# Kernel optimization log

Hardware: AMD Instinct MI355X
Metric: run time of the kernel (lower is better)

The kernel has to match this reference:

```python
import jax, jax.numpy as jnp
import numpy as np

N, D, K = 65536, 256, 4096
EPS = 1e-5
DECAY = 0.99
BN_MOMENTUM = 0.1


def setup_inputs() -> dict:
    key = jax.random.key(0)
    k1, k2, k3, k4, k5, k6 = jax.random.split(key, 6)
    return {
        "x": jax.random.normal(k1, (N, D), dtype=jnp.float32),
        "embedding": jax.random.normal(k2, (K, D), dtype=jnp.float32),
        "ema_cluster_size": jnp.zeros((K,), dtype=jnp.float32),
        "ema_w": jax.random.normal(k3, (K, D), dtype=jnp.float32),
        "running_mean": jax.random.normal(k4, (D,), dtype=jnp.float32) * 0.1,
        "running_var": jax.random.uniform(k5, (D,), dtype=jnp.float32, minval=0.5, maxval=1.5),
    }


def reference(x, embedding, ema_cluster_size, ema_w, running_mean, running_var):
    n_batch = x.shape[0]
    num_embeddings = embedding.shape[0]

    # BatchNorm1d (training mode, affine=False): normalize with batch stats
    mean = jnp.mean(x, axis=0)                       # [D]
    var = jnp.mean((x - mean) ** 2, axis=0)          # biased var, [D]
    xn = (x - mean) / jnp.sqrt(var + EPS)            # [N, D]
    # running stat updates (torch uses unbiased var for running_var)
    new_running_mean = (1.0 - BN_MOMENTUM) * running_mean + BN_MOMENTUM * mean
    var_unbiased = var * (n_batch / (n_batch - 1.0))
    new_running_var = (1.0 - BN_MOMENTUM) * running_var + BN_MOMENTUM * var_unbiased

    # squared euclidean distances [N, K]
    distances = (jnp.sum(xn ** 2, axis=1, keepdims=True)
                 + jnp.sum(embedding ** 2, axis=1)
                 - 2.0 * xn @ embedding.T)
    idx = jnp.argmin(distances, axis=1)              # [N]

    # one-hot scatter stats via segment_sum (== encodings.T contractions)
    counts = jax.ops.segment_sum(jnp.ones((n_batch,), dtype=x.dtype), idx,
                                 num_segments=num_embeddings)   # [K]
    dw = jax.ops.segment_sum(xn, idx, num_segments=num_embeddings)  # [K, D]

    # EMA updates
    new_cs = ema_cluster_size * DECAY + (1.0 - DECAY) * counts
    n_total = jnp.sum(new_cs)
    new_cs = (new_cs + 1e-5) / (n_total + num_embeddings * 1e-5) * n_total
    new_ema_w = ema_w * DECAY + (1.0 - DECAY) * dw
    new_embedding = new_ema_w / new_cs[:, None]

    running_std = jnp.sqrt(new_running_var + EPS)
    embedding_output = new_embedding * running_std[None, :] + new_running_mean[None, :]

    return (idx[:, None], new_embedding, embedding_output, new_cs, new_ema_w,
            new_running_mean, new_running_var)
```

## Files before the change

kernel.cpp:

```cpp
#include <hip/hip_runtime.h>
#include <cfloat>
#include <cmath>

#define NROWS 65536
#define DDIM 256
#define KDIM 4096

typedef short bf16x8 __attribute__((ext_vector_type(8)));
typedef float f32x4 __attribute__((ext_vector_type(4)));

constexpr float EPSV = 1e-5f;
constexpr float DECAYV = 0.99f;
constexpr float MOMV = 0.1f;
constexpr float DELTA = 0.5f;
constexpr int CAP = 16;
constexpr int SEG = 128;

constexpr size_t WS_CNT     = 0;
constexpr size_t WS_NFLAG   = WS_CNT + NROWS;
constexpr size_t WS_HIST    = WS_NFLAG + 64;
constexpr size_t WS_ZEND    = WS_HIST + KDIM;
constexpr size_t WS_START   = WS_ZEND;
constexpr size_t WS_FILLPOS = WS_START + KDIM;
constexpr size_t WS_SEGSTART= WS_FILLPOS + KDIM;
constexpr size_t WS_NSEG    = WS_SEGSTART + KDIM + 64;
constexpr size_t WS_SEGLIST = WS_NSEG + 64;
constexpr size_t WS_PARTSUM = WS_SEGLIST + 4672;
constexpr size_t WS_PARTSQ  = WS_PARTSUM + 2048 * DDIM;
constexpr size_t WS_MIDSUM  = WS_PARTSQ + 2048 * DDIM;
constexpr size_t WS_MIDSQ   = WS_MIDSUM + 256 * DDIM;
constexpr size_t WS_MEAN    = WS_MIDSQ + 256 * DDIM;
constexpr size_t WS_RSTD    = WS_MEAN + DDIM;
constexpr size_t WS_NRMEAN  = WS_RSTD + DDIM;
constexpr size_t WS_NRVAR   = WS_NRMEAN + DDIM;
constexpr size_t WS_BVEC    = WS_NRVAR + DDIM;
constexpr size_t WS_NCSRAW  = WS_BVEC + KDIM;
constexpr size_t WS_NTOT    = WS_NCSRAW + KDIM;
constexpr size_t WS_ROWINFO = WS_NTOT + 64;
constexpr size_t WS_IDX     = WS_ROWINFO + 8 * (size_t)NROWS;
constexpr size_t WS_ROWTHR  = WS_IDX + NROWS;
constexpr size_t WS_FLAG    = WS_ROWTHR + NROWS;
constexpr size_t WS_ROWLIST = WS_FLAG + NROWS;
constexpr size_t WS_CAND    = WS_ROWLIST + NROWS;
constexpr size_t WS_DWPART  = WS_CAND;
constexpr size_t WS_EPROW   = WS_CAND + (size_t)NROWS * CAP;
constexpr size_t WS_EIMG    = WS_EPROW + (size_t)KDIM * DDIM;
constexpr size_t WS_XIMG    = WS_EIMG + 524288;

constexpr size_t O_IDX   = 0;
constexpr size_t O_EMB   = NROWS;
constexpr size_t O_EOUT  = O_EMB + (size_t)KDIM * DDIM;
constexpr size_t O_CS    = O_EOUT + (size_t)KDIM * DDIM;
constexpr size_t O_EMAW  = O_CS + KDIM;
constexpr size_t O_RMEAN = O_EMAW + (size_t)KDIM * DDIM;
constexpr size_t O_RVAR  = O_RMEAN + DDIM;

__device__ inline unsigned bfpack(float a, float b) {
    unsigned ua = __float_as_uint(a), ub = __float_as_uint(b);
    ua = (ua + 0x7FFFu + ((ua >> 16) & 1u)) >> 16;
    ub = (ub + 0x7FFFu + ((ub >> 16) & 1u)) & 0xFFFF0000u;
    return (ua & 0xFFFFu) | ub;
}

__device__ inline float unpackval(float p) {
    return __uint_as_float(__float_as_uint(p) & 0xFFFFF000u);
}

#define GLOAD_LDS16(g, l) __builtin_amdgcn_global_load_lds(                       \
        (const __attribute__((address_space(1))) void*)(g),                        \
        (__attribute__((address_space(3))) void*)(l), 16, 0, 0)

__global__ __launch_bounds__(256) void k_bnpack(const float* __restrict__ x,
                                                float* __restrict__ ws) {
    const int t = threadIdx.x;
    const int q = t & 63, g = t >> 6;
    const int r0 = blockIdx.x * 128 + g * 32;
    char* ximg = (char*)(ws + WS_XIMG);
    const float4* x4 = (const float4*)x;
    float4 s = make_float4(0.f, 0.f, 0.f, 0.f);
    float4 sq = make_float4(0.f, 0.f, 0.f, 0.f);
#pragma unroll 4
    for (int i = 0; i < 32; ++i) {
        const int r = r0 + i;
        const float4 v = x4[(size_t)r * 64 + q];
        s.x += v.x; s.y += v.y; s.z += v.z; s.w += v.w;
        sq.x += v.x * v.x; sq.y += v.y * v.y; sq.z += v.z * v.z; sq.w += v.w * v.w;
        const int db = (8 * q + ((r & 15) << 5)) & 511;
        *(uint2*)(ximg + (size_t)r * 512 + db) = make_uint2(bfpack(v.x, v.y), bfpack(v.z, v.w));
    }
    const size_t p = (size_t)(blockIdx.x * 4 + g) * 64 + q;
    ((float4*)(ws + WS_PARTSUM))[p] = s;
    ((float4*)(ws + WS_PARTSQ))[p]  = sq;
}

__global__ __launch_bounds__(256) void k_bn_mid(float* __restrict__ ws) {
    const int d = threadIdx.x, j = blockIdx.x;
    float s = 0.f, q = 0.f;
#pragma unroll
    for (int i = 0; i < 8; ++i) {
        s += ws[WS_PARTSUM + (size_t)(j * 8 + i) * DDIM + d];
        q += ws[WS_PARTSQ  + (size_t)(j * 8 + i) * DDIM + d];
    }
    ws[WS_MIDSUM + (size_t)j * DDIM + d] = s;
    ws[WS_MIDSQ  + (size_t)j * DDIM + d] = q;
}

__global__ __launch_bounds__(256) void k_bn_final(const float* __restrict__ rmean_in,
                                                  const float* __restrict__ rvar_in,
                                                  float* __restrict__ ws,
                                                  float* __restrict__ out) {
    const int d = threadIdx.x;
    float s = 0.f, sq = 0.f;
    for (int b = 0; b < 256; ++b) {
        s  += ws[WS_MIDSUM + (size_t)b * DDIM + d];
        sq += ws[WS_MIDSQ  + (size_t)b * DDIM + d];
    }
    const float mean = s / (float)NROWS;
    float var = sq / (float)NROWS - mean * mean;
    var = fmaxf(var, 0.f);
    const float rstd = 1.0f / sqrtf(var + EPSV);
    const float nrm  = (1.0f - MOMV) * rmean_in[d] + MOMV * mean;
    const float varu = var * ((float)NROWS / (float)(NROWS - 1));
    const float nrv  = (1.0f - MOMV) * rvar_in[d] + MOMV * varu;
    ws[WS_MEAN + d] = mean;
    ws[WS_RSTD + d] = rstd;
    ws[WS_NRMEAN + d] = nrm;
    ws[WS_NRVAR + d] = nrv;
    out[O_RMEAN + d] = nrm;
    out[O_RVAR + d] = nrv;
}

__global__ __launch_bounds__(256) void k_eprime(const float* __restrict__ emb,
                                                float* __restrict__ ws) {
    const int t = threadIdx.x, l = t & 63, w = t >> 6;
    const int k = blockIdx.x * 4 + w;
    const float4 em = ((const float4*)emb)[(size_t)k * 64 + l];
    const float4 rs = ((const float4*)(ws + WS_RSTD))[l];
    const float4 mn = ((const float4*)(ws + WS_MEAN))[l];
    float4 e;
    e.x = em.x * rs.x; e.y = em.y * rs.y; e.z = em.z * rs.z; e.w = em.w * rs.w;
    ((float4*)(ws + WS_EPROW))[(size_t)k * 64 + l] = e;
    char* img = (char*)(ws + WS_EIMG);
    const int db = (8 * l + ((k & 15) << 5)) & 511;
    *(uint2*)(img + (size_t)k * 512 + db) =
        make_uint2(bfpack(-2.f * e.x, -2.f * e.y), bfpack(-2.f * e.z, -2.f * e.w));
    float red = em.x * em.x + 2.f * mn.x * e.x + em.y * em.y + 2.f * mn.y * e.y
              + em.z * em.z + 2.f * mn.z * e.z + em.w * em.w + 2.f * mn.w * e.w;
    red += __shfl_xor(red, 32); red += __shfl_xor(red, 16); red += __shfl_xor(red, 8);
    red += __shfl_xor(red, 4);  red += __shfl_xor(red, 2);  red += __shfl_xor(red, 1);
    if (l == 0) ws[WS_BVEC + k] = red;
}

__global__ __launch_bounds__(256, 4) void k_gemm_min(float* __restrict__ ws) {
    extern __shared__ char smem[];
    const int t = threadIdx.x, lane = t & 63, w = t >> 6;
    const int l4 = lane & 15, kg = lane >> 4;
    const int tile = blockIdx.x >> 2;
    const int cq   = blockIdx.x & 3;
    const int rowbase = tile * 128 + w * 32;
    const char* ximg = (const char*)(ws + WS_XIMG);
    const char* eimg = (const char*)(ws + WS_EIMG) + (size_t)cq * 524288;
    const float* bvec = ws + WS_BVEC;

    bf16x8 a[2][8];
#pragma unroll
    for (int m = 0; m < 2; ++m) {
        const char* rp = ximg + (size_t)(rowbase + m * 16 + l4) * 512;
#pragma unroll
        for (int ts = 0; ts < 8; ++ts) {
            const int byte = ((kg * 16 + ts * 64) + (l4 << 5)) & 511;
            a[m][ts] = *(const bf16x8*)(rp + byte);
        }
    }

    float b1f[2][4], b2f[2][4];
#pragma unroll
    for (int m = 0; m < 2; ++m)
#pragma unroll
        for (int r = 0; r < 4; ++r) { b1f[m][r] = FLT_MAX; b2f[m][r] = FLT_MAX; }

#pragma unroll
    for (int rr = 0; rr < 4; ++rr) {
        const int off = rr * 4096 + w * 1024;
        GLOAD_LDS16(eimg + off + lane * 16, smem + off);
    }
    float bc0 = bvec[cq * 1024 + l4];
    float bc1 = bvec[cq * 1024 + 16 + l4];
    __syncthreads();

    for (int ch = 0; ch < 32; ++ch) {
        const char* cur = smem + (ch & 1) * 16384;
        float bn0 = 0.f, bn1 = 0.f;
        if (ch + 1 < 32) {
            const char* src = eimg + (size_t)(ch + 1) * 16384;
            char* nb = smem + ((ch + 1) & 1) * 16384;
#pragma unroll
            for (int rr = 0; rr < 4; ++rr) {
                const int off = rr * 4096 + w * 1024;
                GLOAD_LDS16(src + off + lane * 16, nb + off);
            }
            bn0 = bvec[cq * 1024 + (ch + 1) * 32 + l4];
            bn1 = bvec[cq * 1024 + (ch + 1) * 32 + 16 + l4];
        }

        f32x4 acc[2][2];
        acc[0][0] = (f32x4){bc0, bc0, bc0, bc0};
        acc[0][1] = (f32x4){bc1, bc1, bc1, bc1};
        acc[1][0] = acc[0][0];
        acc[1][1] = acc[0][1];

#pragma unroll
        for (int ts = 0; ts < 8; ++ts) {
            const int rot = ((kg * 16 + ts * 64) + (l4 << 5)) & 511;
            bf16x8 bfr[2];
#pragma unroll
            for (int n = 0; n < 2; ++n)
                bfr[n] = *(const bf16x8*)(cur + (n * 16 + l4) * 512 + rot);
#pragma unroll
            for (int m = 0; m < 2; ++m)
#pragma unroll
                for (int n = 0; n < 2; ++n)
                    acc[m][n] = __builtin_amdgcn_mfma_f32_16x16x32_bf16(a[m][ts], bfr[n], acc[m][n], 0, 0, 0);
        }

#pragma unroll
        for (int n = 0; n < 2; ++n) {
            const unsigned col = (unsigned)(cq * 1024 + ch * 32 + n * 16 + l4);
#pragma unroll
            for (int m = 0; m < 2; ++m)
#pragma unroll
                for (int r = 0; r < 4; ++r) {
                    const float p = __uint_as_float(
                        (__float_as_uint(acc[m][n][r]) & 0xFFFFF000u) | col);
                    b2f[m][r] = __builtin_amdgcn_fmed3f(p, b1f[m][r], b2f[m][r]);
                    b1f[m][r] = fminf(p, b1f[m][r]);
                }
        }
        bc0 = bn0; bc1 = bn1;
        __syncthreads();
    }

    float2* rowinfo = (float2*)(ws + WS_ROWINFO);
#pragma unroll
    for (int m = 0; m < 2; ++m)
#pragma unroll
        for (int r = 0; r < 4; ++r) {
            float v1 = b1f[m][r], v2 = b2f[m][r];
#pragma unroll
            for (int st = 1; st < 16; st <<= 1) {
                const float o1 = __shfl_xor(v1, st);
                const float o2 = __shfl_xor(v2, st);
                const float mm = fminf(v2, o2);
                v2 = __builtin_amdgcn_fmed3f(v1, o1, mm);
                v1 = fminf(v1, o1);
            }
            if (l4 == 0) {
                const int row = rowbase + m * 16 + kg * 4 + r;
                rowinfo[(size_t)row * 4 + cq] = make_float2(v1, v2);
            }
        }
}

__global__ __launch_bounds__(256) void k_flag(float* __restrict__ ws,
                                              float* __restrict__ out) {
    const int r = blockIdx.x * 256 + threadIdx.x;
    const float2* rowinfo = (const float2*)(ws + WS_ROWINFO);
    float2 q = rowinfo[(size_t)r * 4];
    float v1 = q.x, v2 = q.y;
#pragma unroll
    for (int c = 1; c < 4; ++c) {
        q = rowinfo[(size_t)r * 4 + c];
        const float mm = fminf(v2, q.y);
        v2 = __builtin_amdgcn_fmed3f(v1, q.x, mm);
        v1 = fminf(v1, q.x);
    }
    const float v1v = unpackval(v1);
    const int   i1  = (int)(__float_as_uint(v1) & 0xFFFu);
    ws[WS_ROWTHR + r] = v1v + DELTA;
    if (unpackval(v2) - v1v <= DELTA) {
        const int pos = atomicAdd((int*)(ws + WS_NFLAG), 1);
        ((int*)(ws + WS_FLAG))[pos] = r;
    } else {
        out[O_IDX + r] = (float)i1;
        ((int*)(ws + WS_IDX))[r] = i1;
        atomicAdd((int*)(ws + WS_HIST) + i1, 1);
    }
}

__global__ __launch_bounds__(256) void k_cand(float* __restrict__ ws) {
    extern __shared__ char smem[];
    const int t = threadIdx.x, lane = t & 63, w = t >> 6;
    const int l4 = lane & 15, kg = lane >> 4;
    const char* ximg = (const char*)(ws + WS_XIMG);
    const char* eimg0 = (const char*)(ws + WS_EIMG);
    const float* bvec = ws + WS_BVEC;
    const int* flag = (const int*)(ws + WS_FLAG);
    int* cnt = (int*)(ws + WS_CNT);
    int* cand = (int*)(ws + WS_CAND);
    const int nflag = *(const int*)(ws + WS_NFLAG);
    if (nflag == 0) return;
    const int ntiles = (nflag + 127) >> 7;
    const int nitems = ntiles * 8;

    for (int item = blockIdx.x; item < nitems; item += gridDim.x) {
        const int tile = item >> 3, slice = item & 7;
        const int base = tile * 128 + w * 32;
        const char* eimg = eimg0 + (size_t)slice * 262144;
        bf16x8 a[2][8];
        int frow[2][4];
        float thr[2][4];
#pragma unroll
        for (int m = 0; m < 2; ++m) {
            const int ia = base + m * 16 + l4;
            const int rowa = flag[ia < nflag ? ia : (nflag - 1)];
            const char* rp = ximg + (size_t)rowa * 512;
#pragma unroll
            for (int ts = 0; ts < 8; ++ts) {
                const int byte = ((kg * 16 + ts * 64) + ((rowa & 15) << 5)) & 511;
                a[m][ts] = *(const bf16x8*)(rp + byte);
            }
#pragma unroll
            for (int r = 0; r < 4; ++r) {
                const int ie = base + m * 16 + kg * 4 + r;
                const bool val = ie < nflag;
                const int rowe = flag[val ? ie : (nflag - 1)];
                frow[m][r] = rowe;
                thr[m][r] = val ? ws[WS_ROWTHR + rowe] : -FLT_MAX;
            }
        }
#pragma unroll
        for (int rr = 0; rr < 4; ++rr) {
            const int off = rr * 4096 + w * 1024;
            GLOAD_LDS16(eimg + off + lane * 16, smem + off);
        }
        __syncthreads();

        for (int ch = 0; ch < 16; ++ch) {
            const char* cur = smem + (ch & 1) * 16384;
            if (ch + 1 < 16) {
                const char* src = eimg + (size_t)(ch + 1) * 16384;
                char* nb = smem + ((ch + 1) & 1) * 16384;
#pragma unroll
                for (int rr = 0; rr < 4; ++rr) {
                    const int off = rr * 4096 + w * 1024;
                    GLOAD_LDS16(src + off + lane * 16, nb + off);
                }
            }
            const float bc0 = bvec[slice * 512 + ch * 32 + l4];
            const float bc1 = bvec[slice * 512 + ch * 32 + 16 + l4];
            f32x4 acc[2][2];
            acc[0][0] = (f32x4){bc0, bc0, bc0, bc0};
            acc[0][1] = (f32x4){bc1, bc1, bc1, bc1};
            acc[1][0] = acc[0][0];
            acc[1][1] = acc[0][1];
#pragma unroll
            for (int ts = 0; ts < 8; ++ts) {
                const int rot = ((kg * 16 + ts * 64) + (l4 << 5)) & 511;
                bf16x8 bfr[2];
#pragma unroll
                for (int n = 0; n < 2; ++n)
                    bfr[n] = *(const bf16x8*)(cur + (n * 16 + l4) * 512 + rot);
#pragma unroll
                for (int m = 0; m < 2; ++m)
#pragma unroll
                    for (int n = 0; n < 2; ++n)
                        acc[m][n] = __builtin_amdgcn_mfma_f32_16x16x32_bf16(a[m][ts], bfr[n], acc[m][n], 0, 0, 0);
            }
#pragma unroll
            for (int n = 0; n < 2; ++n) {
                const int col = slice * 512 + ch * 32 + n * 16 + l4;
#pragma unroll
                for (int m = 0; m < 2; ++m)
#pragma unroll
                    for (int r = 0; r < 4; ++r) {
                        const float s = acc[m][n][r];
                        if (s <= thr[m][r]) {
                            const int rr2 = frow[m][r];
                            const int pos = atomicAdd(&cnt[rr2], 1);
                            if (pos < CAP) cand[(size_t)rr2 * CAP + pos] = col;
                        }
                    }
            }
            __syncthreads();
        }
    }
}

__global__ __launch_bounds__(256) void k_resolve_f(const float* __restrict__ x,
                                                   float* __restrict__ ws,
                                                   float* __restrict__ out) {
    const int t = threadIdx.x, lane = t & 63;
    const int gw = (blockIdx.x * 256 + t) >> 6;
    const int nflag = *(const int*)(ws + WS_NFLAG);
    const int* flag = (const int*)(ws + WS_FLAG);
    const int* cnt = (const int*)(ws + WS_CNT);
    const int* cand = (const int*)(ws + WS_CAND);
    const float* eprow = ws + WS_EPROW;
    const float* bvec = ws + WS_BVEC;
    int* idx_int = (int*)(ws + WS_IDX);
    for (int i = gw; i < nflag; i += 1024) {
        const int row = flag[i];
        const float4 xr = ((const float4*)(x + (size_t)row * DDIM))[lane];
        const int n = cnt[row];
        float bestv = FLT_MAX;
        int bestk = KDIM;
        if (n >= 1 && n <= CAP) {
            for (int c = 0; c < n; ++c) {
                const int k = cand[(size_t)row * CAP + c];
                const float4 er = ((const float4*)(eprow + (size_t)k * DDIM))[lane];
                float p = xr.x * er.x + xr.y * er.y + xr.z * er.z + xr.w * er.w;
                p += __shfl_xor(p, 32); p += __shfl_xor(p, 16); p += __shfl_xor(p, 8);
                p += __shfl_xor(p, 4);  p += __shfl_xor(p, 2);  p += __shfl_xor(p, 1);
                const float s = fmaf(-2.f, p, bvec[k]);
                if (s < bestv || (s == bestv && k < bestk)) { bestv = s; bestk = k; }
            }
        } else {
            for (int k = 0; k < KDIM; ++k) {
                const float4 er = ((const float4*)(eprow + (size_t)k * DDIM))[lane];
                float p = xr.x * er.x + xr.y * er.y + xr.z * er.z + xr.w * er.w;
                p += __shfl_xor(p, 32); p += __shfl_xor(p, 16); p += __shfl_xor(p, 8);
                p += __shfl_xor(p, 4);  p += __shfl_xor(p, 2);  p += __shfl_xor(p, 1);
                const float s = fmaf(-2.f, p, bvec[k]);
                if (s < bestv || (s == bestv && k < bestk)) { bestv = s; bestk = k; }
            }
        }
        if (lane == 0) {
            out[O_IDX + row] = (float)bestk;
            idx_int[row] = bestk;
            atomicAdd((int*)(ws + WS_HIST) + bestk, 1);
        }
    }
}

__global__ __launch_bounds__(256) void k_scan(const float* __restrict__ cs_in,
                                              float* __restrict__ ws) {
    __shared__ int lsum[256], lseg[256];
    __shared__ float redf[256];
    const int t = threadIdx.x;
    const int* hist = (const int*)(ws + WS_HIST);
    int h[16];
    int s = 0, g = 0;
#pragma unroll
    for (int i = 0; i < 16; ++i) {
        h[i] = hist[t * 16 + i];
        s += h[i];
        g += (h[i] + SEG - 1) / SEG;
    }
    lsum[t] = s; lseg[t] = g;
    __syncthreads();
    int v = s, u = g;
    for (int off = 1; off < 256; off <<= 1) {
        const int av = (t >= off) ? lsum[t - off] : 0;
        const int au = (t >= off) ? lseg[t - off] : 0;
        __syncthreads();
        v += av; u += au;
        lsum[t] = v; lseg[t] = u;
        __syncthreads();
    }
    int runs = v - s, rung = u - g;
    int* start = (int*)(ws + WS_START);
    int* fillpos = (int*)(ws + WS_FILLPOS);
    int* segst = (int*)(ws + WS_SEGSTART);
    int* seglist = (int*)(ws + WS_SEGLIST);
    float emapart = 0.f;
#pragma unroll
    for (int i = 0; i < 16; ++i) {
        const int k = t * 16 + i;
        start[k] = runs;
        fillpos[k] = runs;
        segst[k] = rung;
        const int ns = (h[i] + SEG - 1) / SEG;
        for (int j = 0; j < ns; ++j) seglist[rung + j] = (k << 10) | j;
        runs += h[i];
        rung += ns;
        const float ncs = cs_in[k] * DECAYV + (1.0f - DECAYV) * (float)h[i];
        ws[WS_NCSRAW + k] = ncs;
        emapart += ncs;
    }
    if (t == 255) {
        segst[KDIM] = rung;
        *(int*)(ws + WS_NSEG) = rung;
    }
    redf[t] = emapart;
    __syncthreads();
    for (int ss = 128; ss > 0; ss >>= 1) { if (t < ss) redf[t] += redf[t + ss]; __syncthreads(); }
    if (t == 0) ws[WS_NTOT] = redf[0];
}

__global__ __launch_bounds__(256) void k_fill(float* __restrict__ ws) {
    const int r = blockIdx.x * 256 + threadIdx.x;
    const int k = ((const int*)(ws + WS_IDX))[r];
    const int pos = atomicAdd((int*)(ws + WS_FILLPOS) + k, 1);
    ((int*)(ws + WS_ROWLIST))[pos] = r;
}

__global__ __launch_bounds__(256) void k_gather_seg(const float* __restrict__ x,
                                                    float* __restrict__ ws) {
    __shared__ float4 ls[4][64];
    const int b = blockIdx.x;
    if (b >= *(const int*)(ws + WS_NSEG)) return;
    const int e = ((const int*)(ws + WS_SEGLIST))[b];
    const int k = e >> 10, j = e & 1023;
    const int base = ((const int*)(ws + WS_START))[k];
    const int n = ((const int*)(ws + WS_HIST))[k];
    const int st = base + j * SEG;
    const int en = min(st + SEG, base + n);
    const int* rowlist = (const int*)(ws + WS_ROWLIST);
    const int t = threadIdx.x, q = t & 63, g = t >> 6;
    const float4* x4 = (const float4*)x;
    float4 s = make_float4(0.f, 0.f, 0.f, 0.f);
    for (int i = st + g; i < en; i += 4) {
        const float4 v = x4[(size_t)rowlist[i] * 64 + q];
        s.x += v.x; s.y += v.y; s.z += v.z; s.w += v.w;
    }
    ls[g][q] = s;
    __syncthreads();
    if (t < 64) {
        const float4 a0 = ls[0][t], a1 = ls[1][t], a2 = ls[2][t], a3 = ls[3][t];
        float4 r;
        r.x = (a0.x + a1.x) + (a2.x + a3.x);
        r.y = (a0.y + a1.y) + (a2.y + a3.y);
        r.z = (a0.z + a1.z) + (a2.z + a3.z);
        r.w = (a0.w + a1.w) + (a2.w + a3.w);
        ((float4*)(ws + WS_DWPART))[(size_t)b * 64 + t] = r;
    }
}

__global__ __launch_bounds__(64) void k_final(const float* __restrict__ ema_w,
                                              const float* __restrict__ ws,
                                              float* __restrict__ out) {
    const int k = blockIdx.x;
    const int q = threadIdx.x;
    const int* segst = (const int*)(ws + WS_SEGSTART);
    const int ss = segst[k];
    const int ns = segst[k + 1] - ss;
    const float4* dwpart = (const float4*)(ws + WS_DWPART);
    float4 a = make_float4(0.f, 0.f, 0.f, 0.f);
    for (int j = 0; j < ns; ++j) {
        const float4 v = dwpart[(size_t)(ss + j) * 64 + q];
        a.x += v.x; a.y += v.y; a.z += v.z; a.w += v.w;
    }
    const int n = ((const int*)(ws + WS_HIST))[k];
    const float ntot = ws[WS_NTOT];
    const float ncs  = (ws[WS_NCSRAW + k] + 1e-5f) / (ntot + (float)KDIM * 1e-5f) * ntot;
    const float4 mn = ((const float4*)(ws + WS_MEAN))[q];
    const float4 rs = ((const float4*)(ws + WS_RSTD))[q];
    const float4 nrv = ((const float4*)(ws + WS_NRVAR))[q];
    const float4 nrm = ((const float4*)(ws + WS_NRMEAN))[q];
    const float4 ew = ((const float4*)ema_w)[(size_t)k * 64 + q];
    const float fn = (float)n;
    float4 nwv, nembv, eov;
    nwv.x = ew.x * DECAYV + (1.f - DECAYV) * ((a.x - fn * mn.x) * rs.x);
    nwv.y = ew.y * DECAYV + (1.f - DECAYV) * ((a.y - fn * mn.y) * rs.y);
    nwv.z = ew.z * DECAYV + (1.f - DECAYV) * ((a.z - fn * mn.z) * rs.z);
    nwv.w = ew.w * DECAYV + (1.f - DECAYV) * ((a.w - fn * mn.w) * rs.w);
    const float inv = 1.0f / ncs;
    nembv.x = nwv.x * inv; nembv.y = nwv.y * inv;
    nembv.z = nwv.z * inv; nembv.w = nwv.w * inv;
    eov.x = nembv.x * sqrtf(nrv.x + EPSV) + nrm.x;
    eov.y = nembv.y * sqrtf(nrv.y + EPSV) + nrm.y;
    eov.z = nembv.z * sqrtf(nrv.z + EPSV) + nrm.z;
    eov.w = nembv.w * sqrtf(nrv.w + EPSV) + nrm.w;
    ((float4*)(out + O_EMB))[(size_t)k * 64 + q]  = nembv;
    ((float4*)(out + O_EOUT))[(size_t)k * 64 + q] = eov;
    ((float4*)(out + O_EMAW))[(size_t)k * 64 + q] = nwv;
    if (q == 0) out[O_CS + k] = ncs;
}

extern "C" void kernel_launch(void* const* d_in, const int* in_sizes, int n_in,
                              void* d_out, int out_size, void* d_ws, size_t ws_size,
                              hipStream_t stream) {
    const float* x     = (const float*)d_in[0];
    const float* emb   = (const float*)d_in[1];
    const float* cs    = (const float*)d_in[2];
    const float* ema_w = (const float*)d_in[3];
    const float* rmean = (const float*)d_in[4];
    const float* rvar  = (const float*)d_in[5];
    float* out = (float*)d_out;
    float* ws  = (float*)d_ws;

    hipMemsetAsync(ws, 0, WS_ZEND * sizeof(float), stream);

    k_bnpack<<<512, 256, 0, stream>>>(x, ws);
    k_bn_mid<<<256, 256, 0, stream>>>(ws);
    k_bn_final<<<1, 256, 0, stream>>>(rmean, rvar, ws, out);
    k_eprime<<<KDIM / 4, 256, 0, stream>>>(emb, ws);

    constexpr int LDSB = 32768;
    k_gemm_min<<<2048, 256, LDSB, stream>>>(ws);
    k_flag<<<NROWS / 256, 256, 0, stream>>>(ws, out);
    k_cand<<<512, 256, LDSB, stream>>>(ws);
    k_resolve_f<<<256, 256, 0, stream>>>(x, ws, out);

    k_scan<<<1, 256, 0, stream>>>(cs, ws);
    k_fill<<<NROWS / 256, 256, 0, stream>>>(ws);
    k_gather_seg<<<4608, 256, 0, stream>>>(x, ws);
    k_final<<<KDIM, 64, 0, stream>>>(ema_w, ws, out);
}
```

Measured before the change: 308.7 us.

## Read codebook fragments straight from global memory and fold BN partial reduction into pack

The GEMM-argmin kernel no longer double-buffers codebook chunks through LDS with global_load_lds and per-chunk barriers. Each wave now reads its B fragments directly from global memory and relies on cache reuse, and launch bounds drop from 4 to 3 blocks per CU. Separately, the batch-norm partial sums are reduced across the four waves inside k_bnpack through shared memory, so the k_bn_mid launch goes away and k_bn_final sums 512 partials. The trade is removing LDS traffic and synchronization in the GEMM at the risk of higher global/L2 load latency on the hot path, which may stall the MFMAs.

```diff
diff --git a/kernel.cpp b/kernel.cpp
--- a/kernel.cpp
+++ b/kernel.cpp
@@ -26,10 +26,8 @@
 constexpr size_t WS_NSEG    = WS_SEGSTART + KDIM + 64;
 constexpr size_t WS_SEGLIST = WS_NSEG + 64;
 constexpr size_t WS_PARTSUM = WS_SEGLIST + 4672;
-constexpr size_t WS_PARTSQ  = WS_PARTSUM + 2048 * DDIM;
-constexpr size_t WS_MIDSUM  = WS_PARTSQ + 2048 * DDIM;
-constexpr size_t WS_MIDSQ   = WS_MIDSUM + 256 * DDIM;
-constexpr size_t WS_MEAN    = WS_MIDSQ + 256 * DDIM;
+constexpr size_t WS_PARTSQ  = WS_PARTSUM + 512 * DDIM;
+constexpr size_t WS_MEAN    = WS_PARTSQ + 512 * DDIM;
 constexpr size_t WS_RSTD    = WS_MEAN + DDIM;
 constexpr size_t WS_NRMEAN  = WS_RSTD + DDIM;
 constexpr size_t WS_NRVAR   = WS_NRMEAN + DDIM;
@@ -72,6 +70,7 @@
 
 __global__ __launch_bounds__(256) void k_bnpack(const float* __restrict__ x,
                                                 float* __restrict__ ws) {
+    __shared__ float4 lsum[4][64], lsq[4][64];
     const int t = threadIdx.x;
     const int q = t & 63, g = t >> 6;
     const int r0 = blockIdx.x * 128 + g * 32;
@@ -88,21 +87,19 @@
         const int db = (8 * q + ((r & 15) << 5)) & 511;
         *(uint2*)(ximg + (size_t)r * 512 + db) = make_uint2(bfpack(v.x, v.y), bfpack(v.z, v.w));
     }
-    const size_t p = (size_t)(blockIdx.x * 4 + g) * 64 + q;
-    ((float4*)(ws + WS_PARTSUM))[p] = s;
-    ((float4*)(ws + WS_PARTSQ))[p]  = sq;
-}
-
-__global__ __launch_bounds__(256) void k_bn_mid(float* __restrict__ ws) {
-    const int d = threadIdx.x, j = blockIdx.x;
-    float s = 0.f, q = 0.f;
-#pragma unroll
-    for (int i = 0; i < 8; ++i) {
-        s += ws[WS_PARTSUM + (size_t)(j * 8 + i) * DDIM + d];
-        q += ws[WS_PARTSQ  + (size_t)(j * 8 + i) * DDIM + d];
-    }
-    ws[WS_MIDSUM + (size_t)j * DDIM + d] = s;
-    ws[WS_MIDSQ  + (size_t)j * DDIM + d] = q;
+    lsum[g][q] = s; lsq[g][q] = sq;
+    __syncthreads();
+    if (t < 64) {
+        const float4 a0 = lsum[0][t], a1 = lsum[1][t], a2 = lsum[2][t], a3 = lsum[3][t];
+        const float4 b0 = lsq[0][t],  b1 = lsq[1][t],  b2 = lsq[2][t],  b3 = lsq[3][t];
+        float4 S, Q;
+        S.x = (a0.x + a1.x) + (a2.x + a3.x); S.y = (a0.y + a1.y) + (a2.y + a3.y);
+        S.z = (a0.z + a1.z) + (a2.z + a3.z); S.w = (a0.w + a1.w) + (a2.w + a3.w);
+        Q.x = (b0.x + b1.x) + (b2.x + b3.x); Q.y = (b0.y + b1.y) + (b2.y + b3.y);
+        Q.z = (b0.z + b1.z) + (b2.z + b3.z); Q.w = (b0.w + b1.w) + (b2.w + b3.w);
+        ((float4*)(ws + WS_PARTSUM))[(size_t)blockIdx.x * 64 + t] = S;
+        ((float4*)(ws + WS_PARTSQ))[(size_t)blockIdx.x * 64 + t]  = Q;
+    }
 }
 
 __global__ __launch_bounds__(256) void k_bn_final(const float* __restrict__ rmean_in,
@@ -111,9 +108,9 @@
                                                   float* __restrict__ out) {
     const int d = threadIdx.x;
     float s = 0.f, sq = 0.f;
-    for (int b = 0; b < 256; ++b) {
-        s  += ws[WS_MIDSUM + (size_t)b * DDIM + d];
-        sq += ws[WS_MIDSQ  + (size_t)b * DDIM + d];
+    for (int b = 0; b < 512; ++b) {
+        s  += ws[WS_PARTSUM + (size_t)b * DDIM + d];
+        sq += ws[WS_PARTSQ  + (size_t)b * DDIM + d];
     }
     const float mean = s / (float)NROWS;
     float var = sq / (float)NROWS - mean * mean;
@@ -151,12 +148,12 @@
     if (l == 0) ws[WS_BVEC + k] = red;
 }
 
-__global__ __launch_bounds__(256, 4) void k_gemm_min(float* __restrict__ ws) {
-    extern __shared__ char smem[];
-    const int t = threadIdx.x, lane = t & 63, w = t >> 6;
+__global__ __launch_bounds__(256, 3) void k_gemm_min(float* __restrict__ ws) {
+    const int t = threadIdx.x, lane = t & 63;
     const int l4 = lane & 15, kg = lane >> 4;
     const int tile = blockIdx.x >> 2;
     const int cq   = blockIdx.x & 3;
+    const int w = t >> 6;
     const int rowbase = tile * 128 + w * 32;
     const char* ximg = (const char*)(ws + WS_XIMG);
     const char* eimg = (const char*)(ws + WS_EIMG) + (size_t)cq * 524288;
@@ -179,29 +176,10 @@
 #pragma unroll
         for (int r = 0; r < 4; ++r) { b1f[m][r] = FLT_MAX; b2f[m][r] = FLT_MAX; }
 
-#pragma unroll
-    for (int rr = 0; rr < 4; ++rr) {
-        const int off = rr * 4096 + w * 1024;
-        GLOAD_LDS16(eimg + off + lane * 16, smem + off);
-    }
-    float bc0 = bvec[cq * 1024 + l4];
-    float bc1 = bvec[cq * 1024 + 16 + l4];
-    __syncthreads();
-
     for (int ch = 0; ch < 32; ++ch) {
-        const char* cur = smem + (ch & 1) * 16384;
-        float bn0 = 0.f, bn1 = 0.f;
-        if (ch + 1 < 32) {
-            const char* src = eimg + (size_t)(ch + 1) * 16384;
-            char* nb = smem + ((ch + 1) & 1) * 16384;
-#pragma unroll
-            for (int rr = 0; rr < 4; ++rr) {
-                const int off = rr * 4096 + w * 1024;
-                GLOAD_LDS16(src + off + lane * 16, nb + off);
-            }
-            bn0 = bvec[cq * 1024 + (ch + 1) * 32 + l4];
-            bn1 = bvec[cq * 1024 + (ch + 1) * 32 + 16 + l4];
-        }
+        const char* cbase = eimg + (size_t)ch * 16384;
+        const float bc0 = bvec[cq * 1024 + ch * 32 + l4];
+        const float bc1 = bvec[cq * 1024 + ch * 32 + 16 + l4];
 
         f32x4 acc[2][2];
         acc[0][0] = (f32x4){bc0, bc0, bc0, bc0};
@@ -215,7 +193,7 @@
             bf16x8 bfr[2];
 #pragma unroll
             for (int n = 0; n < 2; ++n)
-                bfr[n] = *(const bf16x8*)(cur + (n * 16 + l4) * 512 + rot);
+                bfr[n] = *(const bf16x8*)(cbase + (n * 16 + l4) * 512 + rot);
 #pragma unroll
             for (int m = 0; m < 2; ++m)
 #pragma unroll
@@ -236,8 +214,6 @@
                     b1f[m][r] = fminf(p, b1f[m][r]);
                 }
         }
-        bc0 = bn0; bc1 = bn1;
-        __syncthreads();
     }
 
     float2* rowinfo = (float2*)(ws + WS_ROWINFO);
@@ -582,12 +558,11 @@
     hipMemsetAsync(ws, 0, WS_ZEND * sizeof(float), stream);
 
     k_bnpack<<<512, 256, 0, stream>>>(x, ws);
-    k_bn_mid<<<256, 256, 0, stream>>>(ws);
     k_bn_final<<<1, 256, 0, stream>>>(rmean, rvar, ws, out);
     k_eprime<<<KDIM / 4, 256, 0, stream>>>(emb, ws);
 
     constexpr int LDSB = 32768;
-    k_gemm_min<<<2048, 256, LDSB, stream>>>(ws);
+    k_gemm_min<<<2048, 256, 0, stream>>>(ws);
     k_flag<<<NROWS / 256, 256, 0, stream>>>(ws, out);
     k_cand<<<512, 256, LDSB, stream>>>(ws);
     k_resolve_f<<<256, 256, 0, stream>>>(x, ws, out);
```

After: 498.8 us. 1.62x slower.
